# Kernel optimization log

Measured on AMD Instinct MI355X. Metric: run time of the kernel, lower is better.

The kernel has to match this reference:

```python
import jax, jax.numpy as jnp
import numpy as np

N_E = 1024
E_DIM = 256
BETA = 0.25
BATCH = 131072


def setup_inputs() -> dict:
    key = jax.random.key(0)
    k1, k2 = jax.random.split(key)
    z = jax.random.normal(k1, (BATCH, E_DIM), dtype=jnp.float32)
    # matches nn.Embedding init uniform_(-1/n_e, 1/n_e)
    emb_weight = jax.random.uniform(k2, (N_E, E_DIM), dtype=jnp.float32,
                                    minval=-1.0 / N_E, maxval=1.0 / N_E)
    return {"z": z, "emb_weight": emb_weight}


def reference(z, emb_weight):
    # z: [B, e_dim] (the module's unsqueeze/permute/view is an identity reshape)
    # squared L2 distances: [B, n_e]
    d = (jnp.sum(z * z, axis=1, keepdims=True)
         + jnp.sum(emb_weight * emb_weight, axis=1)
         - 2.0 * jnp.matmul(z, emb_weight.T))
    min_encoding_indices = jnp.argmin(d, axis=1)            # [B]
    min_encodings = jax.nn.one_hot(min_encoding_indices, N_E, dtype=z.dtype)  # [B, n_e]
    z_q = jnp.matmul(min_encodings, emb_weight)             # [B, e_dim]

    sg = jax.lax.stop_gradient
    loss = jnp.mean((sg(z_q) - z) ** 2) + BETA * jnp.mean((z_q - sg(z)) ** 2)

    # straight-through estimator
    z_q_ste = z + sg(z_q - z)

    e_mean = jnp.mean(min_encodings, axis=0)                # [n_e]
    perplexity = jnp.exp(-jnp.sum(e_mean * jnp.log(e_mean + 1e-10)))

    return (z_q_ste, loss, min_encoding_indices[:, None], perplexity)
```

## Files before the change

kernel.cpp:

```cpp
#include <hip/hip_runtime.h>

typedef __attribute__((ext_vector_type(8))) __bf16 bf16x8;
typedef __attribute__((ext_vector_type(4))) float f32x4;
typedef __attribute__((ext_vector_type(8))) unsigned short u16x8;

#define B_ROWS 131072
#define EDIM   256
#define N_E    1024
#define BMR    64
#define CHUNKS 32
#define CAP    16
#define OROWS  32

#define OUT1 ((size_t)B_ROWS * EDIM)
#define OUT2 (OUT1 + 1)
#define OUT3 (OUT2 + B_ROWS)

#define WS_EMBT  0
#define WS_ESQ   524288
#define WS_COUNT 528384
#define WS_LOSS  532480

__device__ __forceinline__ unsigned short f2bf(float f) {
    unsigned u = __float_as_uint(f);
    return (unsigned short)((u + 0x7FFFu + ((u >> 16) & 1u)) >> 16);
}
__device__ __forceinline__ unsigned encf(float f) {
    unsigned u = __float_as_uint(f);
    return u ^ (unsigned)(((int)u >> 31) | 0x80000000);
}
__device__ __forceinline__ float decf(unsigned x) {
    return (x & 0x80000000u) ? __uint_as_float(x ^ 0x80000000u)
                             : __uint_as_float(~x);
}
__device__ __forceinline__ float med3f(float a, float b, float c) {
#if __has_builtin(__builtin_amdgcn_fmed3f)
    return __builtin_amdgcn_fmed3f(a, b, c);
#else
    return fmaxf(fminf(a, b), fminf(fmaxf(a, b), c));
#endif
}

__device__ inline float pw128_sq(const float* p) {
    float4 v0 = *(const float4*)p, v1 = *(const float4*)(p + 4);
    float r[8];
    r[0] = __fmul_rn(v0.x, v0.x); r[1] = __fmul_rn(v0.y, v0.y);
    r[2] = __fmul_rn(v0.z, v0.z); r[3] = __fmul_rn(v0.w, v0.w);
    r[4] = __fmul_rn(v1.x, v1.x); r[5] = __fmul_rn(v1.y, v1.y);
    r[6] = __fmul_rn(v1.z, v1.z); r[7] = __fmul_rn(v1.w, v1.w);
    for (int i = 8; i < 128; i += 8) {
        v0 = *(const float4*)(p + i); v1 = *(const float4*)(p + i + 4);
        r[0] = __fadd_rn(r[0], __fmul_rn(v0.x, v0.x));
        r[1] = __fadd_rn(r[1], __fmul_rn(v0.y, v0.y));
        r[2] = __fadd_rn(r[2], __fmul_rn(v0.z, v0.z));
        r[3] = __fadd_rn(r[3], __fmul_rn(v0.w, v0.w));
        r[4] = __fadd_rn(r[4], __fmul_rn(v1.x, v1.x));
        r[5] = __fadd_rn(r[5], __fmul_rn(v1.y, v1.y));
        r[6] = __fadd_rn(r[6], __fmul_rn(v1.z, v1.z));
        r[7] = __fadd_rn(r[7], __fmul_rn(v1.w, v1.w));
    }
    float s01 = __fadd_rn(r[0], r[1]), s23 = __fadd_rn(r[2], r[3]);
    float s45 = __fadd_rn(r[4], r[5]), s67 = __fadd_rn(r[6], r[7]);
    return __fadd_rn(__fadd_rn(s01, s23), __fadd_rn(s45, s67));
}

__device__ inline float exact_d(const float* zp, const float* ep, float zsq, float eq) {
    const float4* z4 = (const float4*)zp;
    const float4* e4 = (const float4*)ep;
    float acc = 0.f;
#pragma unroll 8
    for (int k = 0; k < 64; ++k) {
        float4 a = z4[k], b = e4[k];
        acc = __fmaf_rn(a.x, b.x, acc);
        acc = __fmaf_rn(a.y, b.y, acc);
        acc = __fmaf_rn(a.z, b.z, acc);
        acc = __fmaf_rn(a.w, b.w, acc);
    }
    return __fsub_rn(__fadd_rn(zsq, eq), 2.0f * acc);
}

__global__ void prep_emb(const float* __restrict__ emb,
                         unsigned short* __restrict__ embT,
                         float* __restrict__ esqg)
{
    int n = blockIdx.x, t = threadIdx.x;
    const float4 v = ((const float4*)(emb + (size_t)n * EDIM))[t];
    ushort4 o = { f2bf(v.x), f2bf(v.y), f2bf(v.z), f2bf(v.w) };
    int g = t >> 1, j0 = (t & 1) * 4;
    *(ushort4*)(embT + ((size_t)g * N_E + n) * 8 + j0) = o;
    if (t < 2) {
        float h = pw128_sq(emb + (size_t)n * EDIM + 128 * t);
        float ho = __shfl_xor(h, 1);
        if (t == 0) esqg[n] = __fadd_rn(h, ho);
    }
}

__global__ __launch_bounds__(256, 2) void vq_search(
    const float* __restrict__ z, const float* __restrict__ emb,
    const unsigned short* __restrict__ embT, const float* __restrict__ esqg,
    float* __restrict__ out, unsigned int* __restrict__ count)
{
    __shared__ float esq_s[N_E];
    __shared__ float zsq_s[BMR], S_s[BMR], thr_s[BMR];
    __shared__ unsigned long long wd64[2][BMR];
    __shared__ unsigned cnt[BMR];
    __shared__ unsigned short list[BMR][CAP];
    __shared__ int rowbest[BMR];
    __shared__ unsigned long long fb4[4];

    const int tid  = threadIdx.x;
    const int blk  = blockIdx.x;
    const int lane = tid & 63;
    const int w    = tid >> 6;
    const int col  = lane & 15;
    const int quad = lane >> 4;
    const int nt   = w >> 1;
    const int mh   = w & 1;

    const float* zb = z + (size_t)blk * BMR * EDIM;

    for (int i = tid; i < N_E; i += 256) esq_s[i] = esqg[i];
    if (tid < BMR) cnt[tid] = 0u;

    bf16x8 afr[2][8];
#pragma unroll
    for (int mti = 0; mti < 2; ++mti) {
        int row = 32 * mh + 16 * mti + col;
#pragma unroll
        for (int ks = 0; ks < 8; ++ks) {
            const float* p = zb + row * EDIM + ((ks * 4 + quad) << 3);
            float4 a0 = *(const float4*)p;
            float4 a1 = *(const float4*)(p + 4);
            u16x8 t = { f2bf(a0.x), f2bf(a0.y), f2bf(a0.z), f2bf(a0.w),
                        f2bf(a1.x), f2bf(a1.y), f2bf(a1.z), f2bf(a1.w) };
            afr[mti][ks] = *(bf16x8*)&t;
        }
    }

    if (tid < 128) {
        int row = tid >> 1, half = tid & 1;
        const float* p = zb + row * EDIM + half * 128;
        float h = pw128_sq(p);
        const float4* p4 = (const float4*)p;
        float4 sv = {0.f, 0.f, 0.f, 0.f};
#pragma unroll
        for (int jj = 0; jj < 32; ++jj) {
            float4 vv = p4[jj];
            sv.x += fabsf(vv.x); sv.y += fabsf(vv.y);
            sv.z += fabsf(vv.z); sv.w += fabsf(vv.w);
        }
        float sa = (sv.x + sv.y) + (sv.z + sv.w);
        float ho = __shfl_xor(h, 1);
        float so = __shfl_xor(sa, 1);
        if (half == 0) {
            zsq_s[row] = __fadd_rn(h, ho);
            S_s[row]   = (sa + so) * 1.001f;
        }
    }
    __syncthreads();

    int koff[8];
#pragma unroll
    for (int ks = 0; ks < 8; ++ks)
        koff[ks] = (((ks * 4 + quad) << 10) + nt * 16 + col) * 8;

    float bd1[2][4], bd2[2][4], bd3[2][4];
    int   cp_[2][4];
#pragma unroll
    for (int mti = 0; mti < 2; ++mti)
#pragma unroll
        for (int r = 0; r < 4; ++r) {
            bd1[mti][r] = INFINITY; bd2[mti][r] = INFINITY; bd3[mti][r] = INFINITY;
            cp_[mti][r] = 0;
        }

#pragma unroll 2
    for (int c = 0; c < CHUNKS; ++c) {
        const unsigned short* cb = embT + (c << 8);
        u16x8 bfr[8];
#pragma unroll
        for (int ks = 0; ks < 8; ++ks)
            bfr[ks] = *(const u16x8*)(cb + koff[ks]);
        f32x4 acc0 = {0.f, 0.f, 0.f, 0.f}, acc1 = {0.f, 0.f, 0.f, 0.f};
#pragma unroll
        for (int ks = 0; ks < 8; ++ks) {
            bf16x8 b = *(bf16x8*)&bfr[ks];
            acc0 = __builtin_amdgcn_mfma_f32_16x16x32_bf16(afr[0][ks], b, acc0, 0, 0, 0);
            acc1 = __builtin_amdgcn_mfma_f32_16x16x32_bf16(afr[1][ks], b, acc1, 0, 0, 0);
        }
        const int codeN = (c << 5) + nt * 16 + col;
        const float eqv = esq_s[codeN];
#pragma unroll
        for (int mti = 0; mti < 2; ++mti)
#pragma unroll
            for (int r = 0; r < 4; ++r) {
                float s = __fmaf_rn(-2.0f, (mti ? acc1[r] : acc0[r]), eqv);
                bool lt1 = s < bd1[mti][r];
                bool lt2 = s < bd2[mti][r];
                bd3[mti][r] = med3f(s, bd2[mti][r], bd3[mti][r]);
                bd2[mti][r] = med3f(s, bd1[mti][r], bd2[mti][r]);
                bd1[mti][r] = fminf(s, bd1[mti][r]);
                int cpo = cp_[mti][r];
                int low = cpo & 0xFFFF;
                cp_[mti][r] = lt1 ? (codeN | (low << 16))
                                  : (lt2 ? (low | (codeN << 16)) : cpo);
            }
    }

#pragma unroll
    for (int mti = 0; mti < 2; ++mti)
#pragma unroll
        for (int r = 0; r < 4; ++r) {
            unsigned long long kk =
                ((unsigned long long)encf(bd1[mti][r]) << 32)
                | (unsigned)(cp_[mti][r] & 0xFFFF);
#pragma unroll
            for (int msk = 1; msk <= 8; msk <<= 1) {
                unsigned long long o = __shfl_xor(kk, msk);
                if (o < kk) kk = o;
            }
            if (col == 0) wd64[nt][32 * mh + 16 * mti + 4 * quad + r] = kk;
        }
    __syncthreads();
    if (tid < BMR) {
        unsigned long long a = wd64[0][tid], b = wd64[1][tid];
        unsigned long long mn = a < b ? a : b;
        thr_s[tid] = decf((unsigned)(mn >> 32)) + (S_s[tid] * (1.0f / 131072.0f) + 1e-4f);
    }
    __syncthreads();

#pragma unroll
    for (int mti = 0; mti < 2; ++mti)
#pragma unroll
        for (int r = 0; r < 4; ++r) {
            int row = 32 * mh + 16 * mti + 4 * quad + r;
            float th = thr_s[row];
            if (__builtin_expect(bd1[mti][r] <= th, 0)) {
                unsigned i = atomicAdd(&cnt[row], 1u);
                if (i < CAP) list[row][i] = (unsigned short)(cp_[mti][r] & 0xFFFF);
            }
            if (__builtin_expect(bd2[mti][r] <= th, 0)) {
                unsigned i = atomicAdd(&cnt[row], 1u);
                if (i < CAP) list[row][i] = (unsigned short)((unsigned)cp_[mti][r] >> 16);
            }
            if (__builtin_expect(bd3[mti][r] <= th, 0))
                atomicAdd(&cnt[row], 1000u);
        }
    __syncthreads();

    {
        int row = tid >> 2, j = tid & 3;
        int cn = (int)cnt[row];
        unsigned long long bkey = ~0ull;
        float zq = zsq_s[row];
        const float* zrow = zb + row * EDIM;
        if (cn <= CAP) {
            for (int i = j; i < cn; i += 4) {
                int n = (int)list[row][i];
                float d = exact_d(zrow, emb + (size_t)n * EDIM, zq, esq_s[n]);
                unsigned long long k2 = ((unsigned long long)encf(d) << 32) | (unsigned)n;
                if (k2 < bkey) bkey = k2;
            }
        }
#pragma unroll
        for (int m = 1; m <= 2; m <<= 1) {
            unsigned long long o = __shfl_xor(bkey, m);
            if (o < bkey) bkey = o;
        }
        if (j == 0) rowbest[row] = (cn <= CAP) ? (int)(bkey & 0xFFFFFFFFu) : -1;
    }
    __syncthreads();

    for (int r = 0; r < BMR; ++r) {
        if (rowbest[r] != -1) continue;
        const float* zr = zb + r * EDIM;
        float zqr = zsq_s[r];
        unsigned long long k = ~0ull;
        for (int ci = 0; ci < 4; ++ci) {
            int n = tid + ci * 256;
            float d = exact_d(zr, emb + (size_t)n * EDIM, zqr, esq_s[n]);
            unsigned long long k2 = ((unsigned long long)encf(d) << 32) | (unsigned)n;
            if (k2 < k) k = k2;
        }
#pragma unroll
        for (int msk = 1; msk <= 32; msk <<= 1) {
            unsigned long long o = __shfl_xor(k, msk);
            if (o < k) k = o;
        }
        if (lane == 0) fb4[w] = k;
        __syncthreads();
        if (tid == 0) {
            unsigned long long m0 = fb4[0] < fb4[1] ? fb4[0] : fb4[1];
            unsigned long long m1 = fb4[2] < fb4[3] ? fb4[2] : fb4[3];
            rowbest[r] = (int)((m0 < m1 ? m0 : m1) & 0xFFFFFFFFu);
        }
        __syncthreads();
    }

    if (tid < BMR) {
        int bn = rowbest[tid];
        out[OUT2 + (size_t)blk * BMR + tid] = (float)bn;
        atomicAdd(&count[bn], 1u);
    }
}

__global__ void vq_output(const float* __restrict__ z, const float* __restrict__ emb,
                          float* __restrict__ out, double* __restrict__ lossSum)
{
    __shared__ double red4s[4];
    const int tid = threadIdx.x;
    const int blk = blockIdx.x;
    const int lane = tid & 63;
    const int w   = tid >> 6;
    const int row = tid >> 3;
    const int q   = tid & 7;
    const size_t grow = (size_t)blk * OROWS + row;
    const int bn = (int)out[OUT2 + grow];
    const float4* zp4 = (const float4*)(z + grow * EDIM);
    const float4* ebr = (const float4*)(emb + (size_t)bn * EDIM);
    float4* outr = (float4*)(out + grow * EDIM);
    double lacc = 0.0;
#pragma unroll
    for (int i = 0; i < 8; ++i) {
        int k4 = q + i * 8;
        float4 zv = zp4[k4];
        float4 ev = ebr[k4];
        float4 o; float sd;
        sd = __fsub_rn(ev.x, zv.x); o.x = __fadd_rn(zv.x, sd); lacc += (double)__fmul_rn(sd, sd);
        sd = __fsub_rn(ev.y, zv.y); o.y = __fadd_rn(zv.y, sd); lacc += (double)__fmul_rn(sd, sd);
        sd = __fsub_rn(ev.z, zv.z); o.z = __fadd_rn(zv.z, sd); lacc += (double)__fmul_rn(sd, sd);
        sd = __fsub_rn(ev.w, zv.w); o.w = __fadd_rn(zv.w, sd); lacc += (double)__fmul_rn(sd, sd);
        outr[k4] = o;
    }
#pragma unroll
    for (int msk = 1; msk <= 32; msk <<= 1) lacc += __shfl_xor(lacc, msk);
    if (lane == 0) red4s[w] = lacc;
    __syncthreads();
    if (tid == 0) atomicAdd(lossSum, red4s[0] + red4s[1] + red4s[2] + red4s[3]);
}

__global__ void vq_finalize(const unsigned int* __restrict__ count,
                            const double* __restrict__ lossSum,
                            float* __restrict__ out)
{
    __shared__ double red[1024];
    int t = threadIdx.x;
    double em = (double)count[t] * (1.0 / 131072.0);
    red[t] = em * log(em + 1e-10);
    __syncthreads();
    for (int s = 512; s > 0; s >>= 1) {
        if (t < s) red[t] += red[t + s];
        __syncthreads();
    }
    if (t == 0) {
        out[OUT3] = (float)exp(-red[0]);
        double m = lossSum[0] * (1.0 / 33554432.0);
        out[OUT1] = (float)(1.25 * m);
    }
}

extern "C" void kernel_launch(void* const* d_in, const int* in_sizes, int n_in,
                              void* d_out, int out_size, void* d_ws, size_t ws_size,
                              hipStream_t stream) {
    const float* z   = (const float*)d_in[0];
    const float* emb = (const float*)d_in[1];
    float* out = (float*)d_out;

    unsigned short* embT = (unsigned short*)((char*)d_ws + WS_EMBT);
    float* esqg          = (float*)((char*)d_ws + WS_ESQ);
    unsigned int* count  = (unsigned int*)((char*)d_ws + WS_COUNT);
    double* lossSum      = (double*)((char*)d_ws + WS_LOSS);

    hipMemsetAsync((char*)d_ws + WS_COUNT, 0, 4104, stream);
    prep_emb<<<N_E, 64, 0, stream>>>(emb, embT, esqg);
    vq_search<<<B_ROWS / BMR, 256, 0, stream>>>(z, emb, embT, esqg, out, count);
    vq_output<<<B_ROWS / OROWS, 256, 0, stream>>>(z, emb, out, lossSum);
    vq_finalize<<<1, 1024, 0, stream>>>(count, lossSum, out);
}
```

Measured before the change: 386.2 us.

## Give each wave all codes for its own 16 rows, removing cross-wave reduction

Each of the four waves now owns 16 rows and scans all 1024 codes in two 16-code halves per chunk. Previously waves split the work as 2 code halves by 2 row halves. The per-row minimum can then be reduced with intra-wave shuffles alone, which drops the wd64 shared buffer, the threshold array and two __syncthreads. Launch bounds rise from 2 to 4 blocks per SIMD because fewer A fragments and accumulators are held in registers. In exchange, each wave loads every embT B fragment itself, so B-operand traffic per wave doubles and the MFMA work gets less reuse of each loaded fragment.

```diff
diff --git a/kernel.cpp b/kernel.cpp
--- a/kernel.cpp
+++ b/kernel.cpp
@@ -95,14 +95,25 @@
     }
 }
 
-__global__ __launch_bounds__(256, 2) void vq_search(
+#define INS(s_, code_, r_)                                                  \
+    {                                                                       \
+        bool lt1 = (s_) < bd1[r_];                                          \
+        bool lt2 = (s_) < bd2[r_];                                          \
+        bd3[r_] = med3f((s_), bd2[r_], bd3[r_]);                            \
+        bd2[r_] = med3f((s_), bd1[r_], bd2[r_]);                            \
+        bd1[r_] = fminf((s_), bd1[r_]);                                     \
+        int low_ = cp_[r_] & 0xFFFF;                                        \
+        cp_[r_] = lt1 ? ((code_) | (low_ << 16))                            \
+                      : (lt2 ? (low_ | ((code_) << 16)) : cp_[r_]);         \
+    }
+
+__global__ __launch_bounds__(256, 4) void vq_search(
     const float* __restrict__ z, const float* __restrict__ emb,
     const unsigned short* __restrict__ embT, const float* __restrict__ esqg,
     float* __restrict__ out, unsigned int* __restrict__ count)
 {
     __shared__ float esq_s[N_E];
-    __shared__ float zsq_s[BMR], S_s[BMR], thr_s[BMR];
-    __shared__ unsigned long long wd64[2][BMR];
+    __shared__ float zsq_s[BMR], S_s[BMR];
     __shared__ unsigned cnt[BMR];
     __shared__ unsigned short list[BMR][CAP];
     __shared__ int rowbest[BMR];
@@ -114,18 +125,16 @@
     const int w    = tid >> 6;
     const int col  = lane & 15;
     const int quad = lane >> 4;
-    const int nt   = w >> 1;
-    const int mh   = w & 1;
+    const int row0 = w * 16;
 
     const float* zb = z + (size_t)blk * BMR * EDIM;
 
     for (int i = tid; i < N_E; i += 256) esq_s[i] = esqg[i];
     if (tid < BMR) cnt[tid] = 0u;
 
-    bf16x8 afr[2][8];
-#pragma unroll
-    for (int mti = 0; mti < 2; ++mti) {
-        int row = 32 * mh + 16 * mti + col;
+    bf16x8 afr[8];
+    {
+        int row = row0 + col;
 #pragma unroll
         for (int ks = 0; ks < 8; ++ks) {
             const float* p = zb + row * EDIM + ((ks * 4 + quad) << 3);
@@ -133,7 +142,7 @@
             float4 a1 = *(const float4*)(p + 4);
             u16x8 t = { f2bf(a0.x), f2bf(a0.y), f2bf(a0.z), f2bf(a0.w),
                         f2bf(a1.x), f2bf(a1.y), f2bf(a1.z), f2bf(a1.w) };
-            afr[mti][ks] = *(bf16x8*)&t;
+            afr[ks] = *(bf16x8*)&t;
         }
     }
 
@@ -162,90 +171,81 @@
     int koff[8];
 #pragma unroll
     for (int ks = 0; ks < 8; ++ks)
-        koff[ks] = (((ks * 4 + quad) << 10) + nt * 16 + col) * 8;
-
-    float bd1[2][4], bd2[2][4], bd3[2][4];
-    int   cp_[2][4];
-#pragma unroll
-    for (int mti = 0; mti < 2; ++mti)
-#pragma unroll
-        for (int r = 0; r < 4; ++r) {
-            bd1[mti][r] = INFINITY; bd2[mti][r] = INFINITY; bd3[mti][r] = INFINITY;
-            cp_[mti][r] = 0;
-        }
-
-#pragma unroll 2
+        koff[ks] = ((((ks * 4 + quad) << 10) + col) << 3);
+
+    float bd1[4], bd2[4], bd3[4];
+    int   cp_[4];
+#pragma unroll
+    for (int r = 0; r < 4; ++r) {
+        bd1[r] = INFINITY; bd2[r] = INFINITY; bd3[r] = INFINITY; cp_[r] = 0;
+    }
+
     for (int c = 0; c < CHUNKS; ++c) {
         const unsigned short* cb = embT + (c << 8);
-        u16x8 bfr[8];
-#pragma unroll
-        for (int ks = 0; ks < 8; ++ks)
-            bfr[ks] = *(const u16x8*)(cb + koff[ks]);
-        f32x4 acc0 = {0.f, 0.f, 0.f, 0.f}, acc1 = {0.f, 0.f, 0.f, 0.f};
-#pragma unroll
-        for (int ks = 0; ks < 8; ++ks) {
-            bf16x8 b = *(bf16x8*)&bfr[ks];
-            acc0 = __builtin_amdgcn_mfma_f32_16x16x32_bf16(afr[0][ks], b, acc0, 0, 0, 0);
-            acc1 = __builtin_amdgcn_mfma_f32_16x16x32_bf16(afr[1][ks], b, acc1, 0, 0, 0);
-        }
-        const int codeN = (c << 5) + nt * 16 + col;
-        const float eqv = esq_s[codeN];
-#pragma unroll
-        for (int mti = 0; mti < 2; ++mti)
+        {
+            u16x8 bfr[8];
+#pragma unroll
+            for (int ks = 0; ks < 8; ++ks)
+                bfr[ks] = *(const u16x8*)(cb + koff[ks]);
+            f32x4 acc = {0.f, 0.f, 0.f, 0.f};
+#pragma unroll
+            for (int ks = 0; ks < 8; ++ks)
+                acc = __builtin_amdgcn_mfma_f32_16x16x32_bf16(afr[ks], *(bf16x8*)&bfr[ks], acc, 0, 0, 0);
+            const int codeN = (c << 5) + col;
+            const float eqv = esq_s[codeN];
 #pragma unroll
             for (int r = 0; r < 4; ++r) {
-                float s = __fmaf_rn(-2.0f, (mti ? acc1[r] : acc0[r]), eqv);
-                bool lt1 = s < bd1[mti][r];
-                bool lt2 = s < bd2[mti][r];
-                bd3[mti][r] = med3f(s, bd2[mti][r], bd3[mti][r]);
-                bd2[mti][r] = med3f(s, bd1[mti][r], bd2[mti][r]);
-                bd1[mti][r] = fminf(s, bd1[mti][r]);
-                int cpo = cp_[mti][r];
-                int low = cpo & 0xFFFF;
-                cp_[mti][r] = lt1 ? (codeN | (low << 16))
-                                  : (lt2 ? (low | (codeN << 16)) : cpo);
+                float s = __fmaf_rn(-2.0f, acc[r], eqv);
+                INS(s, codeN, r);
             }
-    }
-
-#pragma unroll
-    for (int mti = 0; mti < 2; ++mti)
-#pragma unroll
-        for (int r = 0; r < 4; ++r) {
-            unsigned long long kk =
-                ((unsigned long long)encf(bd1[mti][r]) << 32)
-                | (unsigned)(cp_[mti][r] & 0xFFFF);
-#pragma unroll
-            for (int msk = 1; msk <= 8; msk <<= 1) {
-                unsigned long long o = __shfl_xor(kk, msk);
-                if (o < kk) kk = o;
+        }
+        {
+            u16x8 bfr[8];
+#pragma unroll
+            for (int ks = 0; ks < 8; ++ks)
+                bfr[ks] = *(const u16x8*)(cb + koff[ks] + 128);
+            f32x4 acc = {0.f, 0.f, 0.f, 0.f};
+#pragma unroll
+            for (int ks = 0; ks < 8; ++ks)
+                acc = __builtin_amdgcn_mfma_f32_16x16x32_bf16(afr[ks], *(bf16x8*)&bfr[ks], acc, 0, 0, 0);
+            const int codeN = (c << 5) + 16 + col;
+            const float eqv = esq_s[codeN];
+#pragma unroll
+            for (int r = 0; r < 4; ++r) {
+                float s = __fmaf_rn(-2.0f, acc[r], eqv);
+                INS(s, codeN, r);
             }
-            if (col == 0) wd64[nt][32 * mh + 16 * mti + 4 * quad + r] = kk;
-        }
-    __syncthreads();
-    if (tid < BMR) {
-        unsigned long long a = wd64[0][tid], b = wd64[1][tid];
-        unsigned long long mn = a < b ? a : b;
-        thr_s[tid] = decf((unsigned)(mn >> 32)) + (S_s[tid] * (1.0f / 131072.0f) + 1e-4f);
-    }
-    __syncthreads();
-
-#pragma unroll
-    for (int mti = 0; mti < 2; ++mti)
-#pragma unroll
-        for (int r = 0; r < 4; ++r) {
-            int row = 32 * mh + 16 * mti + 4 * quad + r;
-            float th = thr_s[row];
-            if (__builtin_expect(bd1[mti][r] <= th, 0)) {
-                unsigned i = atomicAdd(&cnt[row], 1u);
-                if (i < CAP) list[row][i] = (unsigned short)(cp_[mti][r] & 0xFFFF);
-            }
-            if (__builtin_expect(bd2[mti][r] <= th, 0)) {
-                unsigned i = atomicAdd(&cnt[row], 1u);
-                if (i < CAP) list[row][i] = (unsigned short)((unsigned)cp_[mti][r] >> 16);
-            }
-            if (__builtin_expect(bd3[mti][r] <= th, 0))
-                atomicAdd(&cnt[row], 1000u);
-        }
+        }
+    }
+
+    float th[4];
+#pragma unroll
+    for (int r = 0; r < 4; ++r) {
+        unsigned long long kk =
+            ((unsigned long long)encf(bd1[r]) << 32) | (unsigned)(cp_[r] & 0xFFFF);
+#pragma unroll
+        for (int msk = 1; msk <= 8; msk <<= 1) {
+            unsigned long long o = __shfl_xor(kk, msk);
+            if (o < kk) kk = o;
+        }
+        int row = row0 + quad * 4 + r;
+        th[r] = decf((unsigned)(kk >> 32)) + (S_s[row] * (1.0f / 131072.0f) + 1e-4f);
+    }
+
+#pragma unroll
+    for (int r = 0; r < 4; ++r) {
+        int row = row0 + quad * 4 + r;
+        if (__builtin_expect(bd1[r] <= th[r], 0)) {
+            unsigned i = atomicAdd(&cnt[row], 1u);
+            if (i < CAP) list[row][i] = (unsigned short)(cp_[r] & 0xFFFF);
+        }
+        if (__builtin_expect(bd2[r] <= th[r], 0)) {
+            unsigned i = atomicAdd(&cnt[row], 1u);
+            if (i < CAP) list[row][i] = (unsigned short)((unsigned)cp_[r] >> 16);
+        }
+        if (__builtin_expect(bd3[r] <= th[r], 0))
+            atomicAdd(&cnt[row], 1000u);
+    }
     __syncthreads();
 
     {
```

Measured after the change: 392.2 us. About the same (+1.6%).
